# Kernel optimization log

Measured on AMD Instinct MI355X. Metric: run time of the kernel, lower is better.

Reference implementation:

```python
import jax, jax.numpy as jnp
import numpy as np
from jax import lax

K = 7          # attention window (attn_conv_props.kernel_size)
PAD = K // 2   # 'same' zero padding


def conv1x1(x, W, b):
    # x: (B, Cin, H, W), W: (Cout, Cin), b: (Cout,)
    return jnp.einsum('bchw,oc->bohw', x, W) + b[None, :, None, None]


def unfold(x, k=K):
    # torch Unfold with 'same' zero padding: (B, C, H, W) -> (B, C, k*k, H, W)
    # lax patches are channel-major over the C*k*k feature dim, matching torch.
    B, C, H, W = x.shape
    p = lax.conv_general_dilated_patches(
        x, filter_shape=(k, k), window_strides=(1, 1),
        padding=((PAD, PAD), (PAD, PAD)))
    return p.reshape(B, C, k * k, H, W)


def setup_inputs() -> dict:
    key = jax.random.key(0)
    ks = jax.random.split(key, 8)
    B, Cin, H, W = 2, 128, 64, 64
    heads, dk, dv, Cout = 8, 32, 32, 128
    s_in = 0.02
    return {
        'x':  jax.random.normal(ks[0], (B, Cin, H, W), jnp.float32),
        'Wk': jax.random.normal(ks[1], (heads * dk, Cin), jnp.float32) * s_in,
        'bk': jnp.zeros((heads * dk,), jnp.float32),
        'Wq': jax.random.normal(ks[2], (heads * dk, Cin), jnp.float32) * s_in,
        'bq': jnp.zeros((heads * dk,), jnp.float32),
        'Wv': jax.random.normal(ks[3], (heads * dv, Cin), jnp.float32) * s_in,
        'bv': jnp.zeros((heads * dv,), jnp.float32),
        'Wo': jax.random.normal(ks[4], (Cout, heads * dv), jnp.float32) * s_in,
        'bo': jnp.zeros((Cout,), jnp.float32),
    }


def reference(x, Wk, bk, Wq, bq, Wv, bv, Wo, bo):
    B, Cin, H, W = x.shape
    heads, dk = 8, 32
    dv = 32

    k = conv1x1(x, Wk, bk)   # (B, heads*dk, H, W)
    q = conv1x1(x, Wq, bq)   # (B, heads*dk, H, W)
    v = conv1x1(x, Wv, bv)   # (B, heads*dv, H, W)

    k_unf = unfold(k).reshape(B, heads, dk, K * K, H, W)  # (B,h,dk,A,H,W)
    v_unf = unfold(v).reshape(B, heads, dv, K * K, H, W)  # (B,h,dv,A,H,W)
    q_h = q.reshape(B, heads, dk, H, W)                   # (B,h,dk,H,W)

    scale = jnp.sqrt(jnp.asarray(dk, jnp.float32))
    # per-pixel window logits: (B, h, H, W, A)
    logits = jnp.einsum('bhdxy,bhdaxy->bhxya', q_h, k_unf) / scale
    score = jax.nn.softmax(logits, axis=-1)
    # attend over window: (B, h, dv, H, W)
    attn = jnp.einsum('bhxya,bhdaxy->bhdxy', score, v_unf)
    attn = attn.reshape(B, heads * dv, H, W)

    return conv1x1(attn, Wo, bo)  # (B, Cout, H, W)
```

## Files before the change

kernel.cpp:

```cpp
#include <hip/hip_runtime.h>
#include <hip/hip_bf16.h>
#include <math.h>

constexpr int HW = 4096;

using bf8   = __attribute__((ext_vector_type(8))) short;
using f32x4 = __attribute__((ext_vector_type(4))) float;

constexpr float SCALE = 0.17677669529663687f;


__global__ __launch_bounds__(256) void qkv_fused(
    const float* __restrict__ x,
    const float* __restrict__ Wk, const float* __restrict__ Wq,
    const float* __restrict__ Wv, const float* __restrict__ Wo,
    const float* __restrict__ bk, const float* __restrict__ bq,
    const float* __restrict__ bv,
    unsigned short* __restrict__ Qb, unsigned short* __restrict__ Kc,
    unsigned short* __restrict__ Vc, __hip_bfloat16* __restrict__ Wob)
{
    int bx = blockIdx.x, y = blockIdx.y;
    int t  = threadIdx.x;

    if (bx >= 128) {
        int a    = (bx - 128) * 4 + y;
        int base = a * 256 + t;
        const int STR = 48 * 256;
        for (int i = base; i < 120832; i += STR) {
            int plane = i / 236;
            int c8    = i - plane * 236;
            int byteoff;
            if (c8 < 108) {
                int r6  = c8 / 18;
                int o8  = c8 - r6 * 18;
                int row = r6 < 3 ? r6 : 64 + r6;
                byteoff = row * 160 + o8 * 8;
            } else {
                int s   = c8 - 108;
                int row = 3 + (s >> 1);
                byteoff = row * 160 + ((s & 1) ? 136 : 0);
            }
            *(uint2*)((char*)Vc + (size_t)plane * 11200 + byteoff) = make_uint2(0u, 0u);
        }
        for (int i = base; i < 51456; i += STR) {
            int b   = i >= 25728;
            int r   = i - 25728 * b;
            int pxi = r >> 5;
            int sub = r & 31;
            int yy, xx;
            if (pxi < 420) {
                int r70 = pxi / 70;
                yy = r70 < 3 ? r70 : 64 + r70;
                xx = pxi - r70 * 70;
            } else {
                int q = pxi - 420;
                yy = q / 6 + 3;
                int c6 = q - (yy - 3) * 6;
                xx = c6 < 3 ? c6 : 64 + c6;
            }
            *(uint4*)&Kc[((size_t)b * 4900 + yy * 70 + xx) * 256 + sub * 8] =
                make_uint4(0u, 0u, 0u, 0u);
        }
        for (int i = base; i < 32768; i += STR)
            Wob[i] = __float2bfloat16(Wo[i]);
        return;
    }

    __shared__ __align__(16) unsigned short Xl[8192];
    __shared__ __align__(16) unsigned short Wl[8192];

    int b   = bx >> 6;
    int px0 = bx * 64;
    int hw0 = px0 & 4095;
    int ocl = y * 64;

    {
        int px = t >> 2;
        int q  = t & 3;
        int wv = px >> 4, mm = px & 15;
        const float* xp = x + ((size_t)b * 128 + q * 32) * HW + hw0 + px;
        int dbase = (wv * 4 + q) * 512 + mm * 8;
        #pragma unroll
        for (int kq = 0; kq < 4; ++kq) {
            union { __hip_bfloat16 hh[8]; uint4 u; } pk;
            #pragma unroll
            for (int j = 0; j < 8; ++j)
                pk.hh[j] = __float2bfloat16(xp[(size_t)(kq * 8 + j) * HW]);
            *(uint4*)&Xl[dbase + kq * 128] = pk.u;
        }
    }
    __syncthreads();

    int w = t >> 6, lane = t & 63;
    int m  = lane & 15;
    int kq = lane >> 4;
    int pxw = px0 + w * 16;

    bf8 aF[4];
    #pragma unroll
    for (int ks = 0; ks < 4; ++ks)
        aF[ks] = *(const bf8*)&Xl[(w * 4 + ks) * 512 + lane * 8];

    const float* Wms[3]    = { Wk, Wq, Wv };
    const float* biases[3] = { bk, bq, bv };

    #pragma unroll 1
    for (int s = 0; s < 3; ++s) {
        {
            int oc = t >> 2;
            int q  = t & 3;
            int of = oc >> 4, mo = oc & 15;
            const float* wp = Wms[s] + (size_t)(ocl + oc) * 128 + q * 32;
            int dbw = (of * 4 + q) * 512 + mo * 8;
            #pragma unroll
            for (int kq2 = 0; kq2 < 4; ++kq2) {
                float4 a0 = *(const float4*)(wp + kq2 * 8);
                float4 a1 = *(const float4*)(wp + kq2 * 8 + 4);
                union { __hip_bfloat16 hh[8]; uint4 u; } pk;
                pk.hh[0] = __float2bfloat16(a0.x); pk.hh[1] = __float2bfloat16(a0.y);
                pk.hh[2] = __float2bfloat16(a0.z); pk.hh[3] = __float2bfloat16(a0.w);
                pk.hh[4] = __float2bfloat16(a1.x); pk.hh[5] = __float2bfloat16(a1.y);
                pk.hh[6] = __float2bfloat16(a1.z); pk.hh[7] = __float2bfloat16(a1.w);
                *(uint4*)&Wl[dbw + kq2 * 128] = pk.u;
            }
        }
        __syncthreads();

        f32x4 acc[4] = { {0.f,0.f,0.f,0.f}, {0.f,0.f,0.f,0.f},
                         {0.f,0.f,0.f,0.f}, {0.f,0.f,0.f,0.f} };
        #pragma unroll
        for (int ks = 0; ks < 4; ++ks) {
            #pragma unroll
            for (int of = 0; of < 4; ++of) {
                bf8 bF = *(const bf8*)&Wl[(of * 4 + ks) * 512 + lane * 8];
                acc[of] = __builtin_amdgcn_mfma_f32_16x16x32_bf16(aF[ks], bF, acc[of], 0, 0, 0);
            }
        }

        const float* bias = biases[s];
        if (s == 1) {
            #pragma unroll
            for (int of = 0; of < 4; ++of) {
                float bval = bias[ocl + of * 16 + m];
                #pragma unroll
                for (int r = 0; r < 4; ++r) {
                    int px = pxw + kq * 4 + r;
                    float v = (acc[of][r] + bval) * SCALE;
                    __hip_bfloat16 hv = __float2bfloat16(v);
                    unsigned us = *(unsigned short*)&hv;
                    unsigned un = __shfl_xor((int)us, 1);
                    if (!(m & 1))
                        *(unsigned*)&Qb[(size_t)px * 256 + ocl + of * 16 + m] = us | (un << 16);
                }
            }
        } else if (s == 0) {
            #pragma unroll
            for (int of = 0; of < 4; ++of) {
                float bval = bias[ocl + of * 16 + m];
                #pragma unroll
                for (int r = 0; r < 4; ++r) {
                    int px = pxw + kq * 4 + r;
                    int bb = px >> 12, hw = px & 4095;
                    int yy = hw >> 6, xx = hw & 63;
                    __hip_bfloat16 hv = __float2bfloat16(acc[of][r] + bval);
                    unsigned us = *(unsigned short*)&hv;
                    unsigned un = __shfl_xor((int)us, 1);
                    if (!(m & 1))
                        *(unsigned*)&Kc[((size_t)bb * 4900 + (yy + 3) * 70 + xx + 3) * 256
                                        + ocl + of * 16 + m] = us | (un << 16);
                }
            }
        } else {
            #pragma unroll
            for (int of = 0; of < 4; ++of) {
                float bval = bias[ocl + of * 16 + m];
                int ch = ocl + of * 16 + m;
                union { __hip_bfloat16 h[4]; uint2 u; } pk;
                #pragma unroll
                for (int r = 0; r < 4; ++r)
                    pk.h[r] = __float2bfloat16(acc[of][r] + bval);
                int px = pxw + kq * 4;
                int bb = px >> 12, hw = px & 4095;
                int yy = hw >> 6, xx = hw & 63;
                *(uint2*)&Vc[((size_t)bb * 256 + ch) * 5600 + (yy + 3) * 80 + xx + 4] = pk.u;
            }
        }
        __syncthreads();
    }
}

__global__ __launch_bounds__(512, 4) void attn_proj(
    const unsigned short* __restrict__ Qb, const unsigned short* __restrict__ Kc,
    const unsigned short* __restrict__ Vc, const __hip_bfloat16* __restrict__ Wob,
    const float* __restrict__ bo, float* __restrict__ out)
{
    __shared__ __align__(16) unsigned short P[8 * 2176];
    __shared__ __align__(16) unsigned short AB[16 * 264];

    int id   = blockIdx.x;
    int b    = id >> 8;
    int tile = id & 255;
    int ty0  = (tile >> 3) * 2;
    int tx0  = (tile & 7) * 8;

    int t  = threadIdx.x;
    int w  = t >> 6;
    int l  = t & 63;
    int lr = l & 15;
    int g  = l >> 4;
    int h  = w;

    unsigned short* pw = &P[w * 2176];
    const unsigned short* kcb = Kc + (size_t)b * (4900 * 256) + h * 32 + g * 8;

    int apy = lr >> 3;
    int apx = lr & 7;
    bf8 aQ = *(const bf8*)(Qb +
        ((size_t)b * 4096 + (ty0 + apy) * 64 + tx0 + apx) * 256 + h * 32 + g * 8);

    f32x4 acc[8];
    #pragma unroll
    for (int i = 0; i < 8; ++i) {
        bf8 bK = *(const bf8*)(kcb + ((size_t)(ty0 + i) * 70 + tx0 + lr - 1) * 256);
        f32x4 z = {0.f, 0.f, 0.f, 0.f};
        acc[i] = __builtin_amdgcn_mfma_f32_16x16x32_bf16(aQ, bK, z, 0, 0, 0);
    }

    int gy2 = g >> 1;
    float rsum[4] = {0.f, 0.f, 0.f, 0.f};
    #pragma unroll
    for (int i = 0; i < 8; ++i) {
        bool dyok = ((unsigned)(i - gy2)) <= 6u;
        #pragma unroll
        for (int reg = 0; reg < 4; ++reg) {
            int px_ = ((g & 1) << 2) + reg;
            bool ok = dyok && (((unsigned)(lr - px_ - 1)) <= 6u);
            float e = ok ? __expf(acc[i][reg]) : 0.f;
            rsum[reg] += e;
            __hip_bfloat16 hb = __float2bfloat16(e);
            unsigned us = *(unsigned short*)&hb;
            unsigned un = __shfl_xor((int)us, 1);
            if (!(l & 1))
                *(unsigned*)&pw[(g * 4 + reg) * 136 + i * 16 + lr] = us | (un << 16);
        }
    }
    #pragma unroll
    for (int reg = 0; reg < 4; ++reg) {
        float sm = rsum[reg];
        sm += __shfl_xor(sm, 1);
        sm += __shfl_xor(sm, 2);
        sm += __shfl_xor(sm, 4);
        sm += __shfl_xor(sm, 8);
        rsum[reg] = 1.f / sm;
    }

    f32x4 pv[2] = { {0.f,0.f,0.f,0.f}, {0.f,0.f,0.f,0.f} };
    #pragma unroll
    for (int ks = 0; ks < 4; ++ks) {
        bf8 aP = *(const bf8*)&pw[lr * 136 + ks * 32 + g * 8];
        int yq = 2 * ks + (g >> 1);
        int xv = (g & 1) << 3;
        #pragma unroll
        for (int nt2 = 0; nt2 < 2; ++nt2) {
            bf8 bV = *(const bf8*)(Vc +
                ((size_t)b * 256 + h * 32 + nt2 * 16 + lr) * 5600 +
                (ty0 + yq) * 80 + tx0 + xv);
            pv[nt2] = __builtin_amdgcn_mfma_f32_16x16x32_bf16(aP, bV, pv[nt2], 0, 0, 0);
        }
    }

    #pragma unroll
    for (int nt2 = 0; nt2 < 2; ++nt2) {
        #pragma unroll
        for (int reg = 0; reg < 4; ++reg) {
            float ov = pv[nt2][reg] * rsum[reg];
            __hip_bfloat16 hb = __float2bfloat16(ov);
            unsigned us = *(unsigned short*)&hb;
            unsigned un = __shfl_xor((int)us, 1);
            if (!(l & 1)) {
                int rloc = g * 4 + reg;
                *(unsigned*)&AB[rloc * 264 + h * 32 + nt2 * 16 + lr] = us | (un << 16);
            }
        }
    }
    __syncthreads();

    f32x4 po = {0.f, 0.f, 0.f, 0.f};
    #pragma unroll
    for (int ks = 0; ks < 8; ++ks) {
        bf8 aA = *(const bf8*)&AB[lr * 264 + ks * 32 + g * 8];
        bf8 bF = *(const bf8*)((const unsigned short*)Wob +
                 (size_t)(w * 16 + lr) * 256 + ks * 32 + g * 8);
        po = __builtin_amdgcn_mfma_f32_16x16x32_bf16(aA, bF, po, 0, 0, 0);
    }
    {
        int oc = w * 16 + lr;
        float bval = bo[oc];
        int q_  = g * 4;
        int py  = q_ >> 3;
        int px_ = q_ & 7;
        float4 r4 = make_float4(po[0] + bval, po[1] + bval,
                                po[2] + bval, po[3] + bval);
        *(float4*)&out[((size_t)b * 128 + oc) * 4096 + (ty0 + py) * 64 + tx0 + px_] = r4;
    }
}

extern "C" void kernel_launch(void* const* d_in, const int* in_sizes, int n_in,
                              void* d_out, int out_size, void* d_ws, size_t ws_size,
                              hipStream_t stream) {
    const float* x  = (const float*)d_in[0];
    const float* Wk = (const float*)d_in[1];
    const float* bk = (const float*)d_in[2];
    const float* Wq = (const float*)d_in[3];
    const float* bq = (const float*)d_in[4];
    const float* Wv = (const float*)d_in[5];
    const float* bv = (const float*)d_in[6];
    const float* Wo = (const float*)d_in[7];
    const float* bo = (const float*)d_in[8];
    float* out = (float*)d_out;

    char* wsb = (char*)d_ws;
    unsigned short* Qb  = (unsigned short*)wsb;
    unsigned short* Kc  = (unsigned short*)(wsb + (4u << 20));
    unsigned short* Vc  = (unsigned short*)(wsb + (9u << 20));
    __hip_bfloat16* Wob = (__hip_bfloat16*)(wsb + (15u << 20));

    qkv_fused<<<dim3(140, 4), 256, 0, stream>>>(
        x, Wk, Wq, Wv, Wo, bk, bq, bv, Qb, Kc, Vc, Wob);
    attn_proj<<<dim3(512), 512, 0, stream>>>(Qb, Kc, Vc, Wob, bo, out);
}
```

Baseline: 41.54 us.

## Prefetch weight slices and V fragments early, add MFMA priority and block remap

The QKV kernel's three-stage loop is unrolled so each next weight slice is loaded into registers while the current slice's MFMAs and stores run, hiding global latency behind compute. The attention kernel issues all V fragment loads up front, before the QK MFMAs, rather than inside the PV loop. It also remaps block IDs so neighbouring blocks spread across XCDs, and wraps MFMA sections in s_setprio to favour the matrix units. These changes raise register pressure (extra float4 arrays and V fragments), which may reduce occupancy.

```diff
diff --git a/kernel.cpp b/kernel.cpp
--- a/kernel.cpp
+++ b/kernel.cpp
@@ -9,6 +9,48 @@
 
 constexpr float SCALE = 0.17677669529663687f;
 
+
+__device__ __forceinline__ void load_wslice(const float* Wm, int ocl, int t,
+                                            float4* w8) {
+    int oc = t >> 2, q = t & 3;
+    const float* wp = Wm + (size_t)(ocl + oc) * 128 + q * 32;
+    #pragma unroll
+    for (int k = 0; k < 4; ++k) {
+        w8[2 * k]     = *(const float4*)(wp + k * 8);
+        w8[2 * k + 1] = *(const float4*)(wp + k * 8 + 4);
+    }
+}
+
+__device__ __forceinline__ void pack_wslice(unsigned short* Wl, int t,
+                                            const float4* w8) {
+    int oc = t >> 2, q = t & 3;
+    int of = oc >> 4, mo = oc & 15;
+    int dbw = (of * 4 + q) * 512 + mo * 8;
+    #pragma unroll
+    for (int k = 0; k < 4; ++k) {
+        float4 a0 = w8[2 * k], a1 = w8[2 * k + 1];
+        union { __hip_bfloat16 hh[8]; uint4 u; } pk;
+        pk.hh[0] = __float2bfloat16(a0.x); pk.hh[1] = __float2bfloat16(a0.y);
+        pk.hh[2] = __float2bfloat16(a0.z); pk.hh[3] = __float2bfloat16(a0.w);
+        pk.hh[4] = __float2bfloat16(a1.x); pk.hh[5] = __float2bfloat16(a1.y);
+        pk.hh[6] = __float2bfloat16(a1.z); pk.hh[7] = __float2bfloat16(a1.w);
+        *(uint4*)&Wl[dbw + k * 128] = pk.u;
+    }
+}
+
+__device__ __forceinline__ void do_mfma16(const unsigned short* Wl,
+                                          const bf8* aF, int lane, f32x4* acc) {
+    __builtin_amdgcn_s_setprio(1);
+    #pragma unroll
+    for (int ks = 0; ks < 4; ++ks) {
+        #pragma unroll
+        for (int of = 0; of < 4; ++of) {
+            bf8 bF = *(const bf8*)&Wl[(of * 4 + ks) * 512 + lane * 8];
+            acc[of] = __builtin_amdgcn_mfma_f32_16x16x32_bf16(aF[ks], bF, acc[of], 0, 0, 0);
+        }
+    }
+    __builtin_amdgcn_s_setprio(0);
+}
 
 __global__ __launch_bounds__(256) void qkv_fused(
     const float* __restrict__ x,
@@ -89,6 +131,9 @@
             *(uint4*)&Xl[dbase + kq * 128] = pk.u;
         }
     }
+
+    float4 wA[8], wB[8];
+    load_wslice(Wk, ocl, t, wA);
     __syncthreads();
 
     int w = t >> 6, lane = t & 63;
@@ -101,91 +146,75 @@
     for (int ks = 0; ks < 4; ++ks)
         aF[ks] = *(const bf8*)&Xl[(w * 4 + ks) * 512 + lane * 8];
 
-    const float* Wms[3]    = { Wk, Wq, Wv };
-    const float* biases[3] = { bk, bq, bv };
-
-    #pragma unroll 1
-    for (int s = 0; s < 3; ++s) {
-        {
-            int oc = t >> 2;
-            int q  = t & 3;
-            int of = oc >> 4, mo = oc & 15;
-            const float* wp = Wms[s] + (size_t)(ocl + oc) * 128 + q * 32;
-            int dbw = (of * 4 + q) * 512 + mo * 8;
-            #pragma unroll
-            for (int kq2 = 0; kq2 < 4; ++kq2) {
-                float4 a0 = *(const float4*)(wp + kq2 * 8);
-                float4 a1 = *(const float4*)(wp + kq2 * 8 + 4);
-                union { __hip_bfloat16 hh[8]; uint4 u; } pk;
-                pk.hh[0] = __float2bfloat16(a0.x); pk.hh[1] = __float2bfloat16(a0.y);
-                pk.hh[2] = __float2bfloat16(a0.z); pk.hh[3] = __float2bfloat16(a0.w);
-                pk.hh[4] = __float2bfloat16(a1.x); pk.hh[5] = __float2bfloat16(a1.y);
-                pk.hh[6] = __float2bfloat16(a1.z); pk.hh[7] = __float2bfloat16(a1.w);
-                *(uint4*)&Wl[dbw + kq2 * 128] = pk.u;
-            }
-        }
-        __syncthreads();
-
+    pack_wslice(Wl, t, wA);
+    __syncthreads();
+    load_wslice(Wq, ocl, t, wB);
+    {
         f32x4 acc[4] = { {0.f,0.f,0.f,0.f}, {0.f,0.f,0.f,0.f},
                          {0.f,0.f,0.f,0.f}, {0.f,0.f,0.f,0.f} };
-        #pragma unroll
-        for (int ks = 0; ks < 4; ++ks) {
+        do_mfma16(Wl, aF, lane, acc);
+        #pragma unroll
+        for (int of = 0; of < 4; ++of) {
+            float bval = bk[ocl + of * 16 + m];
             #pragma unroll
-            for (int of = 0; of < 4; ++of) {
-                bf8 bF = *(const bf8*)&Wl[(of * 4 + ks) * 512 + lane * 8];
-                acc[of] = __builtin_amdgcn_mfma_f32_16x16x32_bf16(aF[ks], bF, acc[of], 0, 0, 0);
-            }
-        }
-
-        const float* bias = biases[s];
-        if (s == 1) {
-            #pragma unroll
-            for (int of = 0; of < 4; ++of) {
-                float bval = bias[ocl + of * 16 + m];
-                #pragma unroll
-                for (int r = 0; r < 4; ++r) {
-                    int px = pxw + kq * 4 + r;
-                    float v = (acc[of][r] + bval) * SCALE;
-                    __hip_bfloat16 hv = __float2bfloat16(v);
-                    unsigned us = *(unsigned short*)&hv;
-                    unsigned un = __shfl_xor((int)us, 1);
-                    if (!(m & 1))
-                        *(unsigned*)&Qb[(size_t)px * 256 + ocl + of * 16 + m] = us | (un << 16);
-                }
-            }
-        } else if (s == 0) {
-            #pragma unroll
-            for (int of = 0; of < 4; ++of) {
-                float bval = bias[ocl + of * 16 + m];
-                #pragma unroll
-                for (int r = 0; r < 4; ++r) {
-                    int px = pxw + kq * 4 + r;
-                    int bb = px >> 12, hw = px & 4095;
-                    int yy = hw >> 6, xx = hw & 63;
-                    __hip_bfloat16 hv = __float2bfloat16(acc[of][r] + bval);
-                    unsigned us = *(unsigned short*)&hv;
-                    unsigned un = __shfl_xor((int)us, 1);
-                    if (!(m & 1))
-                        *(unsigned*)&Kc[((size_t)bb * 4900 + (yy + 3) * 70 + xx + 3) * 256
-                                        + ocl + of * 16 + m] = us | (un << 16);
-                }
-            }
-        } else {
-            #pragma unroll
-            for (int of = 0; of < 4; ++of) {
-                float bval = bias[ocl + of * 16 + m];
-                int ch = ocl + of * 16 + m;
-                union { __hip_bfloat16 h[4]; uint2 u; } pk;
-                #pragma unroll
-                for (int r = 0; r < 4; ++r)
-                    pk.h[r] = __float2bfloat16(acc[of][r] + bval);
-                int px = pxw + kq * 4;
+            for (int r = 0; r < 4; ++r) {
+                int px = pxw + kq * 4 + r;
                 int bb = px >> 12, hw = px & 4095;
                 int yy = hw >> 6, xx = hw & 63;
-                *(uint2*)&Vc[((size_t)bb * 256 + ch) * 5600 + (yy + 3) * 80 + xx + 4] = pk.u;
-            }
-        }
-        __syncthreads();
+                __hip_bfloat16 hv = __float2bfloat16(acc[of][r] + bval);
+                unsigned us = *(unsigned short*)&hv;
+                unsigned un = __shfl_xor((int)us, 1);
+                if (!(m & 1))
+                    *(unsigned*)&Kc[((size_t)bb * 4900 + (yy + 3) * 70 + xx + 3) * 256
+                                    + ocl + of * 16 + m] = us | (un << 16);
+            }
+        }
+    }
+    __syncthreads();
+
+    pack_wslice(Wl, t, wB);
+    __syncthreads();
+    load_wslice(Wv, ocl, t, wA);
+    {
+        f32x4 acc[4] = { {0.f,0.f,0.f,0.f}, {0.f,0.f,0.f,0.f},
+                         {0.f,0.f,0.f,0.f}, {0.f,0.f,0.f,0.f} };
+        do_mfma16(Wl, aF, lane, acc);
+        #pragma unroll
+        for (int of = 0; of < 4; ++of) {
+            float bval = bq[ocl + of * 16 + m];
+            #pragma unroll
+            for (int r = 0; r < 4; ++r) {
+                int px = pxw + kq * 4 + r;
+                float v = (acc[of][r] + bval) * SCALE;
+                __hip_bfloat16 hv = __float2bfloat16(v);
+                unsigned us = *(unsigned short*)&hv;
+                unsigned un = __shfl_xor((int)us, 1);
+                if (!(m & 1))
+                    *(unsigned*)&Qb[(size_t)px * 256 + ocl + of * 16 + m] = us | (un << 16);
+            }
+        }
+    }
+    __syncthreads();
+
+    pack_wslice(Wl, t, wA);
+    __syncthreads();
+    {
+        f32x4 acc[4] = { {0.f,0.f,0.f,0.f}, {0.f,0.f,0.f,0.f},
+                         {0.f,0.f,0.f,0.f}, {0.f,0.f,0.f,0.f} };
+        do_mfma16(Wl, aF, lane, acc);
+        #pragma unroll
+        for (int of = 0; of < 4; ++of) {
+            float bval = bv[ocl + of * 16 + m];
+            int ch = ocl + of * 16 + m;
+            union { __hip_bfloat16 h[4]; uint2 u; } pk;
+            #pragma unroll
+            for (int r = 0; r < 4; ++r)
+                pk.h[r] = __float2bfloat16(acc[of][r] + bval);
+            int px = pxw + kq * 4;
+            int bb = px >> 12, hw = px & 4095;
+            int yy = hw >> 6, xx = hw & 63;
+            *(uint2*)&Vc[((size_t)bb * 256 + ch) * 5600 + (yy + 3) * 80 + xx + 4] = pk.u;
+        }
     }
 }
 
@@ -197,7 +226,9 @@
     __shared__ __align__(16) unsigned short P[8 * 2176];
     __shared__ __align__(16) unsigned short AB[16 * 264];
 
-    int id   = blockIdx.x;
+    int bid = blockIdx.x;
+    int id  = (bid & 7) * 64 + (bid >> 3);
+
     int b    = id >> 8;
     int tile = id & 255;
     int ty0  = (tile >> 3) * 2;
@@ -218,13 +249,27 @@
     bf8 aQ = *(const bf8*)(Qb +
         ((size_t)b * 4096 + (ty0 + apy) * 64 + tx0 + apx) * 256 + h * 32 + g * 8);
 
+    bf8 vF[4][2];
+    #pragma unroll
+    for (int ks = 0; ks < 4; ++ks) {
+        int yq = 2 * ks + (g >> 1);
+        int xv = (g & 1) << 3;
+        #pragma unroll
+        for (int nt2 = 0; nt2 < 2; ++nt2)
+            vF[ks][nt2] = *(const bf8*)(Vc +
+                ((size_t)b * 256 + h * 32 + nt2 * 16 + lr) * 5600 +
+                (ty0 + yq) * 80 + tx0 + xv);
+    }
+
     f32x4 acc[8];
+    __builtin_amdgcn_s_setprio(1);
     #pragma unroll
     for (int i = 0; i < 8; ++i) {
         bf8 bK = *(const bf8*)(kcb + ((size_t)(ty0 + i) * 70 + tx0 + lr - 1) * 256);
         f32x4 z = {0.f, 0.f, 0.f, 0.f};
         acc[i] = __builtin_amdgcn_mfma_f32_16x16x32_bf16(aQ, bK, z, 0, 0, 0);
     }
+    __builtin_amdgcn_s_setprio(0);
 
     int gy2 = g >> 1;
     float rsum[4] = {0.f, 0.f, 0.f, 0.f};
@@ -255,19 +300,15 @@
     }
 
     f32x4 pv[2] = { {0.f,0.f,0.f,0.f}, {0.f,0.f,0.f,0.f} };
+    __builtin_amdgcn_s_setprio(1);
     #pragma unroll
     for (int ks = 0; ks < 4; ++ks) {
         bf8 aP = *(const bf8*)&pw[lr * 136 + ks * 32 + g * 8];
-        int yq = 2 * ks + (g >> 1);
-        int xv = (g & 1) << 3;
-        #pragma unroll
-        for (int nt2 = 0; nt2 < 2; ++nt2) {
-            bf8 bV = *(const bf8*)(Vc +
-                ((size_t)b * 256 + h * 32 + nt2 * 16 + lr) * 5600 +
-                (ty0 + yq) * 80 + tx0 + xv);
-            pv[nt2] = __builtin_amdgcn_mfma_f32_16x16x32_bf16(aP, bV, pv[nt2], 0, 0, 0);
-        }
-    }
+        #pragma unroll
+        for (int nt2 = 0; nt2 < 2; ++nt2)
+            pv[nt2] = __builtin_amdgcn_mfma_f32_16x16x32_bf16(aP, vF[ks][nt2], pv[nt2], 0, 0, 0);
+    }
+    __builtin_amdgcn_s_setprio(0);
 
     #pragma unroll
     for (int nt2 = 0; nt2 < 2; ++nt2) {
@@ -286,6 +327,7 @@
     __syncthreads();
 
     f32x4 po = {0.f, 0.f, 0.f, 0.f};
+    __builtin_amdgcn_s_setprio(1);
     #pragma unroll
     for (int ks = 0; ks < 8; ++ks) {
         bf8 aA = *(const bf8*)&AB[lr * 264 + ks * 32 + g * 8];
@@ -293,6 +335,7 @@
                  (size_t)(w * 16 + lr) * 256 + ks * 32 + g * 8);
         po = __builtin_amdgcn_mfma_f32_16x16x32_bf16(aA, bF, po, 0, 0, 0);
     }
+    __builtin_amdgcn_s_setprio(0);
     {
         int oc = w * 16 + lr;
         float bval = bo[oc];
```

After: 42.38 us. +2.0%, slower.
